# Performance work log

Measured on AMD Instinct MI355X. Metric: run time of the kernel, lower is better.

Reference implementation:

```python
import jax, jax.numpy as jnp
import numpy as np

DIM = 1024
H = 4          # index_heads
D_I = 32       # index_dim
EXP = 2        # gate_mlp_expansion -> hidden = H*EXP = 8
MAX_REL = 128
NUM_BUCKETS = 2 * MAX_REL + 1
N_Q, N_K = 2048, 4096


def setup_inputs() -> dict:
    key = jax.random.key(0)
    ks = jax.random.split(key, 12)
    hidden = H * EXP
    inp = {
        "query_states": jax.random.normal(ks[0], (N_Q, DIM), dtype=jnp.float32),
        "key_states": jax.random.normal(ks[1], (N_K, DIM), dtype=jnp.float32),
        "query_pos": jnp.sort(jax.random.randint(ks[2], (N_Q,), 0, 8192)),
        "key_pos": jnp.sort(jax.random.randint(ks[3], (N_K,), 0, 8192)),
        # parameters (torch nn.Linear convention: y = x @ W.T + b)
        "Wq": jax.random.normal(ks[4], (2 * H * D_I, DIM), dtype=jnp.float32) * (1.0 / np.sqrt(DIM)),
        "Wk": jax.random.normal(ks[5], (2 * H * D_I, DIM), dtype=jnp.float32) * (1.0 / np.sqrt(DIM)),
        "rpe_table": jax.random.normal(ks[6], (NUM_BUCKETS, H), dtype=jnp.float32) * 0.02,
        "gate_w1": jax.random.normal(ks[7], (hidden, H), dtype=jnp.float32) * 0.5,
        "gate_b1": jnp.zeros((hidden,), dtype=jnp.float32),
        "gate_w2": jax.random.normal(ks[8], (H, hidden), dtype=jnp.float32) * 0.5,
        "gate_b2": jnp.zeros((H,), dtype=jnp.float32),
    }
    return inp


def reference(query_states, key_states, query_pos, key_pos,
              Wq, Wk, rpe_table, gate_w1, gate_b1, gate_w2, gate_b2):
    # projections: [N, 2H, D_i]
    q = (query_states @ Wq.T).reshape(N_Q, 2 * H, D_I)
    k = (key_states @ Wk.T).reshape(N_K, 2 * H, D_I)
    # batched dot product over all 2H heads: [N_q, N_k, 2H]
    dot = jnp.einsum('qhd,khd->qkh', q, k)
    dot_data, dot_gate = dot[..., :H], dot[..., H:]
    # learned RPE bias via bucketed gather: [N_q, N_k, H]
    rel = query_pos[:, None] - key_pos[None, :]
    bucket = jnp.clip(rel, -MAX_REL, MAX_REL) + MAX_REL
    rpe = rpe_table[bucket]
    # data stream
    relu_scores = jax.nn.relu(dot_data + rpe)
    # gate stream: tiny MLP over head dim, then sigmoid
    g_in = dot_gate + rpe
    g_hid = jax.nn.relu(jnp.einsum('qkh,eh->qke', g_in, gate_w1) + gate_b1)
    gate = jax.nn.sigmoid(jnp.einsum('qke,he->qkh', g_hid, gate_w2) + gate_b2)
    # gated scores summed over heads: [N_q, N_k]
    return (relu_scores * gate).sum(axis=-1)
```

## Files before the change

### kernel.cpp

```cpp
#include <hip/hip_runtime.h>
#include <hip/hip_fp16.h>

#define NQ 2048
#define NK 4096
#define DIMK 1024
#define HD 256
#define NBUCKET 257

typedef _Float16 h4 __attribute__((ext_vector_type(4)));
typedef float f4 __attribute__((ext_vector_type(4)));

#define GLDS16(gp, lp)                                              \
  __builtin_amdgcn_global_load_lds(                                 \
      (const __attribute__((address_space(1))) void*)(gp),          \
      (__attribute__((address_space(3))) void*)(lp), 16, 0, 0)

__global__ __launch_bounds__(256) void proj_kernel(
    const float* __restrict__ Xq, const float* __restrict__ Xk,
    const float* __restrict__ Wq, const float* __restrict__ Wk,
    _Float16* __restrict__ Pq, _Float16* __restrict__ Pk)
{
  __shared__ __align__(16) float xs[2][32 * 64];
  __shared__ __align__(16) float wsh[2][64 * 64];

  const int t = threadIdx.x;
  const int lane = t & 63;
  const int wave = t >> 6;
  const int bx = blockIdx.x;
  const bool isq = bx < (NQ / 32);
  const float* __restrict__ X = isq ? Xq : Xk;
  const float* __restrict__ W = isq ? Wq : Wk;
  _Float16* __restrict__ P = isq ? Pq : Pk;
  const int rb = (isq ? bx : bx - NQ / 32) * 32;
  const int cb = blockIdx.y * 64;
  const int r15 = lane & 15, g = lane >> 4;
  const int wq = wave >> 1, wk = wave & 1;
  const int c4 = t & 15;

  f4 acc[2];
  acc[0] = (f4){0.f, 0.f, 0.f, 0.f};
  acc[1] = (f4){0.f, 0.f, 0.f, 0.f};

  auto stage = [&](int buf, int kb) {
#pragma unroll
    for (int c = 0; c < 2; ++c) {
      int flat = c * 1024 + t * 4;
      int row = flat >> 6;
      int gc = c4 ^ (row & 7);
      GLDS16(X + (size_t)(rb + row) * DIMK + kb + gc * 4, &xs[buf][flat]);
    }
#pragma unroll
    for (int c = 0; c < 4; ++c) {
      int flat = c * 1024 + t * 4;
      int row = flat >> 6;
      int gc = c4 ^ (row & 7);
      GLDS16(W + (size_t)(cb + row) * DIMK + kb + gc * 4, &wsh[buf][flat]);
    }
  };

  auto compute = [&](int buf) {
    const int arow = wq * 16 + r15;
#pragma unroll
    for (int kc = 0; kc < 4; ++kc) {
      int k4 = kc * 4 + g;
      f4 af = *(const f4*)&xs[buf][arow * 64 + ((k4 ^ (arow & 7)) << 2)];
      h4 a;
      a[0] = (_Float16)af[0]; a[1] = (_Float16)af[1];
      a[2] = (_Float16)af[2]; a[3] = (_Float16)af[3];
#pragma unroll
      for (int cs = 0; cs < 2; ++cs) {
        int brow = wk * 32 + cs * 16 + r15;
        f4 bf = *(const f4*)&wsh[buf][brow * 64 + ((k4 ^ (brow & 7)) << 2)];
        h4 b;
        b[0] = (_Float16)bf[0]; b[1] = (_Float16)bf[1];
        b[2] = (_Float16)bf[2]; b[3] = (_Float16)bf[3];
        acc[cs] = __builtin_amdgcn_mfma_f32_16x16x16f16(a, b, acc[cs], 0, 0, 0);
      }
    }
  };

  stage(0, 0);
  __syncthreads();
  int buf = 0;
  for (int tt = 0; tt < DIMK / 64; ++tt) {
    if (tt + 1 < DIMK / 64) stage(buf ^ 1, (tt + 1) * 64);
    compute(buf);
    __syncthreads();
    buf ^= 1;
  }

#pragma unroll
  for (int cs = 0; cs < 2; ++cs)
#pragma unroll
    for (int i = 0; i < 4; ++i)
      P[(size_t)(rb + wq * 16 + g * 4 + i) * HD + cb + wk * 32 + cs * 16 + r15] =
          (_Float16)acc[cs][i];
}

__global__ __launch_bounds__(256) void fused_kernel(
    const _Float16* __restrict__ qp, const _Float16* __restrict__ kp,
    const int* __restrict__ qpos, const int* __restrict__ kpos,
    const float* __restrict__ rpe, const float* __restrict__ gw1,
    const float* __restrict__ gb1, const float* __restrict__ gw2,
    const float* __restrict__ gb2, float* __restrict__ out)
{
  __shared__ __align__(16) _Float16 qlds[32 * 256];
  __shared__ __align__(16) _Float16 klds[64 * 256];
  __shared__ __align__(16) float rpel[NBUCKET * 4];
  __shared__ int qposl[32];
  __shared__ int kposl[64];

  const int t = threadIdx.x;
  const int lane = t & 63, wave = t >> 6;
  const int wq = wave >> 1, wk = wave & 1;
  const int qb = blockIdx.y * 32, kb = blockIdx.x * 64;
  const int r15 = lane & 15, g = lane >> 4;

  for (int i = t; i < NBUCKET * 4; i += 256) rpel[i] = rpe[i];
  if (t < 32) qposl[t] = qpos[qb + t];
  else if (t < 96) kposl[t - 32] = kpos[kb + t - 32];

#pragma unroll
  for (int j = 0; j < 4; ++j) {
    int idx = t + j * 256;
    int row = idx >> 5, c = idx & 31;
    *(uint4*)&qlds[row * 256 + ((c * 8) ^ ((row & 7) << 3))] =
        *(const uint4*)(qp + (size_t)(qb + row) * HD + c * 8);
  }
#pragma unroll
  for (int j = 0; j < 8; ++j) {
    int idx = t + j * 256;
    int row = idx >> 5, c = idx & 31;
    *(uint4*)&klds[row * 256 + ((c * 8) ^ ((row & 7) << 3))] =
        *(const uint4*)(kp + (size_t)(kb + row) * HD + c * 8);
  }
  __syncthreads();

  f4 acc[2][8];
#pragma unroll
  for (int s = 0; s < 2; ++s)
#pragma unroll
    for (int h = 0; h < 8; ++h) acc[s][h] = (f4){0.f, 0.f, 0.f, 0.f};

  const int qrow = wq * 16 + r15;
#pragma unroll
  for (int h = 0; h < 8; ++h) {
#pragma unroll
    for (int c = 0; c < 2; ++c) {
      int colh = h * 32 + c * 16 + g * 4;
      h4 a = *(const h4*)&qlds[qrow * 256 + (colh ^ ((r15 & 7) << 3))];
#pragma unroll
      for (int s = 0; s < 2; ++s) {
        int krow = wk * 32 + s * 16 + r15;
        h4 b = *(const h4*)&klds[krow * 256 + (colh ^ ((r15 & 7) << 3))];
        acc[s][h] = __builtin_amdgcn_mfma_f32_16x16x16f16(a, b, acc[s][h], 0, 0, 0);
      }
    }
  }

  float w1v[8][4], b1v[8], w2v[4][8], b2v[4];
#pragma unroll
  for (int e = 0; e < 8; ++e) {
    b1v[e] = gb1[e];
#pragma unroll
    for (int h = 0; h < 4; ++h) w1v[e][h] = gw1[e * 4 + h];
  }
#pragma unroll
  for (int h = 0; h < 4; ++h) {
    b2v[h] = gb2[h];
#pragma unroll
    for (int e = 0; e < 8; ++e) w2v[h][e] = gw2[h * 8 + e];
  }

#pragma unroll
  for (int s = 0; s < 2; ++s) {
    const int kl = wk * 32 + s * 16 + r15;
    const int kpv = kposl[kl];
#pragma unroll
    for (int i = 0; i < 4; ++i) {
      const int ql = wq * 16 + g * 4 + i;
      int rel = qposl[ql] - kpv;
      int bidx = rel < -128 ? -128 : (rel > 128 ? 128 : rel);
      bidx += 128;
      f4 rp = *(const f4*)&rpel[bidx * 4];

      float sd[4], gi[4];
#pragma unroll
      for (int h = 0; h < 4; ++h) {
        sd[h] = fmaxf(acc[s][h][i] + rp[h], 0.0f);
        gi[h] = acc[s][4 + h][i] + rp[h];
      }
      float gs[4];
#pragma unroll
      for (int h = 0; h < 4; ++h) gs[h] = b2v[h];
#pragma unroll
      for (int e = 0; e < 8; ++e) {
        float he = b1v[e];
#pragma unroll
        for (int h = 0; h < 4; ++h) he += gi[h] * w1v[e][h];
        he = fmaxf(he, 0.0f);
#pragma unroll
        for (int h = 0; h < 4; ++h) gs[h] += he * w2v[h][e];
      }
      float ov = 0.0f;
#pragma unroll
      for (int h = 0; h < 4; ++h) {
        float sg = __builtin_amdgcn_rcpf(1.0f + __expf(-gs[h]));
        ov += sd[h] * sg;
      }
      out[(size_t)(qb + ql) * NK + kb + kl] = ov;
    }
  }
}

extern "C" void kernel_launch(void* const* d_in, const int* in_sizes, int n_in,
                              void* d_out, int out_size, void* d_ws, size_t ws_size,
                              hipStream_t stream) {
  const float* Xq  = (const float*)d_in[0];
  const float* Xk  = (const float*)d_in[1];
  const int*   qpos = (const int*)d_in[2];
  const int*   kpos = (const int*)d_in[3];
  const float* Wq  = (const float*)d_in[4];
  const float* Wk  = (const float*)d_in[5];
  const float* rpe = (const float*)d_in[6];
  const float* gw1 = (const float*)d_in[7];
  const float* gb1 = (const float*)d_in[8];
  const float* gw2 = (const float*)d_in[9];
  const float* gb2 = (const float*)d_in[10];
  float* out = (float*)d_out;

  _Float16* qpf = (_Float16*)d_ws;
  _Float16* kpf = qpf + (size_t)NQ * HD;

  proj_kernel<<<dim3(NQ / 32 + NK / 32, 4), 256, 0, stream>>>(
      Xq, Xk, Wq, Wk, qpf, kpf);
  fused_kernel<<<dim3(NK / 64, NQ / 32), 256, 0, stream>>>(
      qpf, kpf, qpos, kpos, rpe, gw1, gb1, gw2, gb2, out);
}
```

Before: 57.97 us.

## Load MFMA fragments directly from global and run gate MLP in packed fp16

Drops the Q/K shared-memory staging in the fused kernel: each wave loads its A fragments into registers once and streams B fragments from global per 16-row slab, accumulating only 8 tiles at a time instead of 16. The gate MLP is rewritten with packed half2 arithmetic, and the sigmoid now uses exp2 directly. Launch bounds request 4 blocks per SM for occupancy. The aim is less LDS traffic, fewer synchronisations and fewer VALU ops in the epilogue, at the cost of uncoalesced global fragment loads and reduced precision in the gate computation.

Result: slower. 113.6 us (+95.9%).

```diff
diff --git a/kernel.cpp b/kernel.cpp
--- a/kernel.cpp
+++ b/kernel.cpp
@@ -7,6 +7,7 @@
 #define HD 256
 #define NBUCKET 257
 
+typedef _Float16 h2 __attribute__((ext_vector_type(2)));
 typedef _Float16 h4 __attribute__((ext_vector_type(4)));
 typedef float f4 __attribute__((ext_vector_type(4)));
 
@@ -97,18 +98,14 @@
           (_Float16)acc[cs][i];
 }
 
-__global__ __launch_bounds__(256) void fused_kernel(
+__global__ __launch_bounds__(256, 4) void fused_kernel(
     const _Float16* __restrict__ qp, const _Float16* __restrict__ kp,
     const int* __restrict__ qpos, const int* __restrict__ kpos,
     const float* __restrict__ rpe, const float* __restrict__ gw1,
     const float* __restrict__ gb1, const float* __restrict__ gw2,
     const float* __restrict__ gb2, float* __restrict__ out)
 {
-  __shared__ __align__(16) _Float16 qlds[32 * 256];
-  __shared__ __align__(16) _Float16 klds[64 * 256];
   __shared__ __align__(16) float rpel[NBUCKET * 4];
-  __shared__ int qposl[32];
-  __shared__ int kposl[64];
 
   const int t = threadIdx.x;
   const int lane = t & 63, wave = t >> 6;
@@ -117,98 +114,92 @@
   const int r15 = lane & 15, g = lane >> 4;
 
   for (int i = t; i < NBUCKET * 4; i += 256) rpel[i] = rpe[i];
-  if (t < 32) qposl[t] = qpos[qb + t];
-  else if (t < 96) kposl[t - 32] = kpos[kb + t - 32];
-
+  __syncthreads();
+
+  const int qrow = qb + wq * 16 + r15;
+  const _Float16* qbase = qp + (size_t)qrow * HD + g * 4;
+  h4 afr[8][2];
+#pragma unroll
+  for (int h = 0; h < 8; ++h)
+#pragma unroll
+    for (int c = 0; c < 2; ++c)
+      afr[h][c] = *(const h4*)(qbase + h * 32 + c * 16);
+
+  h2 w1p[4][4], b1p[4];
+  h2 w2p[8][2], b2p[2];
 #pragma unroll
   for (int j = 0; j < 4; ++j) {
-    int idx = t + j * 256;
-    int row = idx >> 5, c = idx & 31;
-    *(uint4*)&qlds[row * 256 + ((c * 8) ^ ((row & 7) << 3))] =
-        *(const uint4*)(qp + (size_t)(qb + row) * HD + c * 8);
+    b1p[j] = (h2){(_Float16)gb1[2 * j], (_Float16)gb1[2 * j + 1]};
+#pragma unroll
+    for (int h = 0; h < 4; ++h)
+      w1p[h][j] = (h2){(_Float16)gw1[(2 * j) * 4 + h],
+                       (_Float16)gw1[(2 * j + 1) * 4 + h]};
   }
 #pragma unroll
-  for (int j = 0; j < 8; ++j) {
-    int idx = t + j * 256;
-    int row = idx >> 5, c = idx & 31;
-    *(uint4*)&klds[row * 256 + ((c * 8) ^ ((row & 7) << 3))] =
-        *(const uint4*)(kp + (size_t)(kb + row) * HD + c * 8);
-  }
-  __syncthreads();
-
-  f4 acc[2][8];
-#pragma unroll
-  for (int s = 0; s < 2; ++s)
-#pragma unroll
-    for (int h = 0; h < 8; ++h) acc[s][h] = (f4){0.f, 0.f, 0.f, 0.f};
-
-  const int qrow = wq * 16 + r15;
-#pragma unroll
-  for (int h = 0; h < 8; ++h) {
-#pragma unroll
-    for (int c = 0; c < 2; ++c) {
-      int colh = h * 32 + c * 16 + g * 4;
-      h4 a = *(const h4*)&qlds[qrow * 256 + (colh ^ ((r15 & 7) << 3))];
-#pragma unroll
-      for (int s = 0; s < 2; ++s) {
-        int krow = wk * 32 + s * 16 + r15;
-        h4 b = *(const h4*)&klds[krow * 256 + (colh ^ ((r15 & 7) << 3))];
-        acc[s][h] = __builtin_amdgcn_mfma_f32_16x16x16f16(a, b, acc[s][h], 0, 0, 0);
-      }
-    }
-  }
-
-  float w1v[8][4], b1v[8], w2v[4][8], b2v[4];
-#pragma unroll
-  for (int e = 0; e < 8; ++e) {
-    b1v[e] = gb1[e];
-#pragma unroll
-    for (int h = 0; h < 4; ++h) w1v[e][h] = gw1[e * 4 + h];
-  }
-#pragma unroll
-  for (int h = 0; h < 4; ++h) {
-    b2v[h] = gb2[h];
-#pragma unroll
-    for (int e = 0; e < 8; ++e) w2v[h][e] = gw2[h * 8 + e];
-  }
+  for (int j = 0; j < 2; ++j)
+    b2p[j] = (h2){(_Float16)gb2[2 * j], (_Float16)gb2[2 * j + 1]};
+#pragma unroll
+  for (int e = 0; e < 8; ++e)
+#pragma unroll
+    for (int j = 0; j < 2; ++j)
+      w2p[e][j] = (h2){(_Float16)gw2[(2 * j) * 8 + e],
+                       (_Float16)gw2[(2 * j + 1) * 8 + e]};
+
+  const int4 qp4 = *(const int4*)(qpos + qb + wq * 16 + g * 4);
 
 #pragma unroll
   for (int s = 0; s < 2; ++s) {
-    const int kl = wk * 32 + s * 16 + r15;
-    const int kpv = kposl[kl];
+    const int krow = kb + wk * 32 + s * 16 + r15;
+    const _Float16* kbase = kp + (size_t)krow * HD + g * 4;
+
+    f4 acc[8];
+#pragma unroll
+    for (int h = 0; h < 8; ++h) acc[h] = (f4){0.f, 0.f, 0.f, 0.f};
+#pragma unroll
+    for (int h = 0; h < 8; ++h)
+#pragma unroll
+      for (int c = 0; c < 2; ++c) {
+        h4 b = *(const h4*)(kbase + h * 32 + c * 16);
+        acc[h] = __builtin_amdgcn_mfma_f32_16x16x16f16(afr[h][c], b, acc[h], 0, 0, 0);
+      }
+
+    const int kpv = kpos[krow];
 #pragma unroll
     for (int i = 0; i < 4; ++i) {
-      const int ql = wq * 16 + g * 4 + i;
-      int rel = qposl[ql] - kpv;
-      int bidx = rel < -128 ? -128 : (rel > 128 ? 128 : rel);
-      bidx += 128;
+      int rel = qp4[i] - kpv;
+      int bidx = (rel < -128 ? -128 : (rel > 128 ? 128 : rel)) + 128;
       f4 rp = *(const f4*)&rpel[bidx * 4];
 
-      float sd[4], gi[4];
+      h2 gi01 = (h2){(_Float16)(acc[4][i] + rp[0]), (_Float16)(acc[5][i] + rp[1])};
+      h2 gi23 = (h2){(_Float16)(acc[6][i] + rp[2]), (_Float16)(acc[7][i] + rp[3])};
+
+      h2 hid[4];
+#pragma unroll
+      for (int j = 0; j < 4; ++j) {
+        h2 a = b1p[j];
+        a += (h2){gi01[0], gi01[0]} * w1p[0][j];
+        a += (h2){gi01[1], gi01[1]} * w1p[1][j];
+        a += (h2){gi23[0], gi23[0]} * w1p[2][j];
+        a += (h2){gi23[1], gi23[1]} * w1p[3][j];
+        hid[j] = __builtin_elementwise_max(a, (h2)(_Float16)0.0f);
+      }
+      h2 gs0 = b2p[0], gs1 = b2p[1];
+#pragma unroll
+      for (int e = 0; e < 8; ++e) {
+        h2 he = (h2){hid[e >> 1][e & 1], hid[e >> 1][e & 1]};
+        gs0 += he * w2p[e][0];
+        gs1 += he * w2p[e][1];
+      }
+
+      float ov = 0.0f;
 #pragma unroll
       for (int h = 0; h < 4; ++h) {
-        sd[h] = fmaxf(acc[s][h][i] + rp[h], 0.0f);
-        gi[h] = acc[s][4 + h][i] + rp[h];
-      }
-      float gs[4];
-#pragma unroll
-      for (int h = 0; h < 4; ++h) gs[h] = b2v[h];
-#pragma unroll
-      for (int e = 0; e < 8; ++e) {
-        float he = b1v[e];
-#pragma unroll
-        for (int h = 0; h < 4; ++h) he += gi[h] * w1v[e][h];
-        he = fmaxf(he, 0.0f);
-#pragma unroll
-        for (int h = 0; h < 4; ++h) gs[h] += he * w2v[h][e];
-      }
-      float ov = 0.0f;
-#pragma unroll
-      for (int h = 0; h < 4; ++h) {
-        float sg = __builtin_amdgcn_rcpf(1.0f + __expf(-gs[h]));
-        ov += sd[h] * sg;
-      }
-      out[(size_t)(qb + ql) * NK + kb + kl] = ov;
+        float gsf = (float)((h < 2 ? gs0 : gs1)[h & 1]);
+        float sd = fmaxf(acc[h][i] + rp[h], 0.0f);
+        float e2 = __builtin_amdgcn_exp2f(gsf * -1.44269504f);
+        ov += sd * __builtin_amdgcn_rcpf(1.0f + e2);
+      }
+      out[(size_t)(qb + wq * 16 + g * 4 + i) * NK + krow] = ov;
     }
   }
 }
```
